# Optimization experiments

Hardware: AMD Instinct MI355X
Metric: run time of the kernel (lower is better)

The kernel has to match this reference:

```python
import jax, jax.numpy as jnp
import numpy as np

N_NODES = 100000
N_EDGES = 1600000
IN_C, HID_C, OUT_C = 128, 128, 64


def setup_inputs() -> dict:
    key = jax.random.key(0)
    k = jax.random.split(key, 5)
    x = jax.random.normal(k[0], (N_NODES, IN_C), dtype=jnp.float32)
    edge_index = jax.random.randint(k[1], (2, N_EDGES), 0, N_NODES, dtype=jnp.int32)
    # Glorot-ish scaling for the GCNConv linear weights
    W1 = jax.random.normal(k[2], (IN_C, HID_C), dtype=jnp.float32) * (1.0 / np.sqrt(IN_C))
    b1 = jnp.zeros((HID_C,), dtype=jnp.float32)
    W2 = jax.random.normal(k[3], (HID_C, OUT_C), dtype=jnp.float32) * (1.0 / np.sqrt(HID_C))
    b2 = jnp.zeros((OUT_C,), dtype=jnp.float32)
    return {"x": x, "edge_index": edge_index, "W1": W1, "b1": b1, "W2": W2, "b2": b2}


def _gcn_conv(h, W, b, src, dst, deg_inv_sqrt, n):
    # h: [N, F_in] -> linear transform, then deg-normalized scatter-add over edges
    h = h @ W  # [N, F_out]
    norm = deg_inv_sqrt[src] * deg_inv_sqrt[dst]  # [E+N] (self-loops included)
    msgs = h[src] * norm[:, None]  # gather + scale
    out = jax.ops.segment_sum(msgs, dst, num_segments=n)  # scatter-add to dst
    return out + b


def reference(x, edge_index, W1, b1, W2, b2):
    n = x.shape[0]
    loops = jnp.arange(n, dtype=edge_index.dtype)
    src = jnp.concatenate([edge_index[0], loops])  # add self-loops (PyG default)
    dst = jnp.concatenate([edge_index[1], loops])
    deg = jax.ops.segment_sum(jnp.ones_like(dst, dtype=x.dtype), dst, num_segments=n)
    deg_inv_sqrt = jax.lax.rsqrt(deg)  # deg >= 1 due to self-loops

    h = _gcn_conv(x, W1, b1, src, dst, deg_inv_sqrt, n)
    h = jax.nn.relu(h)
    # F.dropout(training=False) is identity at inference
    h = _gcn_conv(h, W2, b2, src, dst, deg_inv_sqrt, n)
    return jax.nn.log_softmax(h, axis=1)
```

## Files before the change

### kernel.cpp

```cpp
#include <hip/hip_runtime.h>
#include <hip/hip_bf16.h>


typedef unsigned short ushortT;
typedef unsigned char ucharT;
typedef __attribute__((ext_vector_type(8))) short short8v;
typedef __attribute__((ext_vector_type(4))) float float4v;
typedef __attribute__((ext_vector_type(2))) float float2v;
typedef __attribute__((ext_vector_type(8))) unsigned short ushort8v;

__device__ __forceinline__ float bf2f(ushortT u) {
  union { unsigned int i; float f; } x;
  x.i = ((unsigned int)u) << 16;
  return x.f;
}

__device__ __forceinline__ ushortT f2bf(float f) {
  __hip_bfloat16 h = __float2bfloat16(f);
  return *(ushortT*)&h;
}

__device__ __forceinline__ ucharT f2fp8(float f) {
  unsigned int w = __builtin_amdgcn_cvt_pk_fp8_f32(f, f, 0, false);
  return (ucharT)(w & 0xff);
}

__device__ __forceinline__ void fp8x8_to_f32(unsigned int lo, unsigned int hi,
                                             float* f) {
  float2v p0 = __builtin_amdgcn_cvt_pk_f32_fp8(lo, false);
  float2v p1 = __builtin_amdgcn_cvt_pk_f32_fp8(lo, true);
  float2v p2 = __builtin_amdgcn_cvt_pk_f32_fp8(hi, false);
  float2v p3 = __builtin_amdgcn_cvt_pk_f32_fp8(hi, true);
  f[0] = p0[0]; f[1] = p0[1]; f[2] = p1[0]; f[3] = p1[1];
  f[4] = p2[0]; f[5] = p2[1]; f[6] = p3[0]; f[7] = p3[1];
}

__device__ __forceinline__ void fp8x4_to_f32(unsigned int w, float* f) {
  float2v p0 = __builtin_amdgcn_cvt_pk_f32_fp8(w, false);
  float2v p1 = __builtin_amdgcn_cvt_pk_f32_fp8(w, true);
  f[0] = p0[0]; f[1] = p0[1]; f[2] = p1[0]; f[3] = p1[1];
}

__device__ __forceinline__ bool probe_isbf(const void* xv) {
  const ushortT* xr = (const ushortT*)xv;
  const int lane = threadIdx.x & 63;
  float v = bf2f(xr[lane]);
  bool sane = isfinite(v) && fabsf(v) < 1e4f;
  return __ballot(sane) == ~0ull;
}

__global__ __launch_bounds__(256) void bhist_k(const int* __restrict__ dst, int E, int B,
                                               int* __restrict__ gbc,
                                               const void* __restrict__ W1v,
                                               const void* __restrict__ W2v,
                                               const void* __restrict__ xv,
                                               ushortT* __restrict__ Wt1,
                                               ushortT* __restrict__ Wt2) {
  __shared__ int h[512];
  const int tid = threadIdx.x;
  const int gi = blockIdx.x * 256 + tid;
  if (gi < 24576) {
    const bool isbf = probe_isbf(xv);
    if (gi < 16384) {
      int nn = gi & 127, k = gi >> 7;
      ushortT v = isbf ? ((const ushortT*)W1v)[k * 128 + nn]
                       : f2bf(((const float*)W1v)[k * 128 + nn]);
      Wt1[nn * 128 + k] = v;
    } else {
      int j = gi - 16384;
      int nn = j & 63, k = j >> 6;
      ushortT v = isbf ? ((const ushortT*)W2v)[k * 64 + nn]
                       : f2bf(((const float*)W2v)[k * 64 + nn]);
      Wt2[nn * 128 + k] = v;
    }
  }
  for (int i = tid; i < B; i += 256) h[i] = 0;
  __syncthreads();
  const int i0 = blockIdx.x * 8192;
  const int iend = min(i0 + 8192, E);
  for (int i = i0 + tid; i < iend; i += 256) atomicAdd(&h[dst[i] >> 8], 1);
  __syncthreads();
  for (int i = tid; i < B; i += 256)
    if (h[i]) atomicAdd(&gbc[i], h[i]);
}

__global__ __launch_bounds__(256) void bscan_k(const int* __restrict__ gbc, int B,
                                               int* __restrict__ bbase,
                                               int* __restrict__ gcur) {
  __shared__ int p[256];
  const int t = threadIdx.x;
  int a = (2 * t < B) ? gbc[2 * t] : 0;
  int b = (2 * t + 1 < B) ? gbc[2 * t + 1] : 0;
  const int sum = a + b;
  p[t] = sum;
  __syncthreads();
  int run = sum;
  for (int off = 1; off < 256; off <<= 1) {
    int v = (t >= off) ? p[t - off] : 0;
    __syncthreads();
    run += v;
    p[t] = run;
    __syncthreads();
  }
  const int excl = run - sum;
  if (2 * t < B) { bbase[2 * t] = excl; gcur[2 * t] = excl; }
  if (2 * t + 1 < B) { bbase[2 * t + 1] = excl + a; gcur[2 * t + 1] = excl + a; }
}

__global__ __launch_bounds__(256) void bin_k(const int* __restrict__ srcv,
                                             const int* __restrict__ dstv, int E, int B,
                                             int* __restrict__ gcur,
                                             int* __restrict__ tmp) {
  __shared__ int hist[512];
  __shared__ int base[512];
  const int tid = threadIdx.x;
  const int i0 = blockIdx.x * 8192;
  const int iend = min(i0 + 8192, E);
  for (int i = tid; i < B; i += 256) hist[i] = 0;
  __syncthreads();
  for (int i = i0 + tid; i < iend; i += 256) atomicAdd(&hist[dstv[i] >> 8], 1);
  __syncthreads();
  for (int i = tid; i < B; i += 256) {
    int h = hist[i];
    base[i] = h ? atomicAdd(&gcur[i], h) : 0;
    hist[i] = 0;
  }
  __syncthreads();
  for (int i = i0 + tid; i < iend; i += 256) {
    int d = dstv[i];
    int s = srcv[i];
    int b = d >> 8;
    int l = atomicAdd(&hist[b], 1);
    tmp[base[b] + l] = s | ((d & 255) << 17);
  }
}

__global__ __launch_bounds__(256) void csr_k(const int* __restrict__ tmp,
                                             const int* __restrict__ bbase,
                                             const int* __restrict__ gbc, int n,
                                             int2* __restrict__ rpc,
                                             float* __restrict__ dis,
                                             int* __restrict__ col) {
  __shared__ int lhist[256];
  __shared__ int lexcl[256];
  const int b = blockIdx.x;
  const int tid = threadIdx.x;
  const int e0 = bbase[b];
  const int e1 = e0 + gbc[b];
  lhist[tid] = 0;
  __syncthreads();
  for (int i = e0 + tid; i < e1; i += 256) atomicAdd(&lhist[tmp[i] >> 17], 1);
  __syncthreads();
  const int v = lhist[tid];
  int run = v;
  lexcl[tid] = run;
  __syncthreads();
  for (int off = 1; off < 256; off <<= 1) {
    int t = (tid >= off) ? lexcl[tid - off] : 0;
    __syncthreads();
    run += t;
    lexcl[tid] = run;
    __syncthreads();
  }
  const int excl = run - v;
  const int node = (b << 8) + tid;
  if (node < n) {
    rpc[node] = make_int2(e0 + excl, v);
    dis[node] = rsqrtf((float)(v + 1));
  }
  lhist[tid] = 0;
  lexcl[tid] = excl;
  __syncthreads();
  for (int i = e0 + tid; i < e1; i += 256) {
    int p = tmp[i];
    int dloc = p >> 17;
    int s = p & 131071;
    int l = atomicAdd(&lhist[dloc], 1);
    col[e0 + lexcl[dloc] + l] = s;
  }
}

__global__ __launch_bounds__(512) void gemm1_k(const void* __restrict__ xv,
                                               const ushortT* __restrict__ Wt1,
                                               const float* __restrict__ dis,
                                               ucharT* __restrict__ Hb8, int n) {
  __shared__ ushortT sW[128 * 132];
  const bool isbf = probe_isbf(xv);
  const int tid = threadIdx.x;
  for (int i = tid; i < 4096; i += 512) {
    int nn = i >> 5, k4 = (i & 31) * 4;
    *(ushort4*)&sW[nn * 132 + k4] = *(const ushort4*)&Wt1[nn * 128 + k4];
  }
  __syncthreads();

  const int wave = tid >> 6;
  const int lane = tid & 63;
  const int m = lane & 15;
  const int quad = lane >> 4;
  const int row = blockIdx.x * 128 + wave * 16 + m;
  const int rowc = min(row, n - 1);

  float4v acc[8];
#pragma unroll
  for (int t = 0; t < 8; ++t) acc[t] = (float4v)(0.f);

  if (isbf) {
    const ushortT* xp = (const ushortT*)xv + (size_t)rowc * 128 + quad * 8;
#pragma unroll
    for (int kc = 0; kc < 4; ++kc) {
      short8v af = *(const short8v*)(xp + kc * 32);
#pragma unroll
      for (int nb = 0; nb < 8; ++nb) {
        short8v bf = *(const short8v*)&sW[(nb * 16 + m) * 132 + kc * 32 + quad * 8];
        acc[nb] = __builtin_amdgcn_mfma_f32_16x16x32_bf16(af, bf, acc[nb], 0, 0, 0);
      }
    }
  } else {
    const float* xp = (const float*)xv + (size_t)rowc * 128 + quad * 8;
#pragma unroll
    for (int kc = 0; kc < 4; ++kc) {
      float4 lo = *(const float4*)(xp + kc * 32);
      float4 hi = *(const float4*)(xp + kc * 32 + 4);
      short8v af;
      af[0] = (short)f2bf(lo.x); af[1] = (short)f2bf(lo.y);
      af[2] = (short)f2bf(lo.z); af[3] = (short)f2bf(lo.w);
      af[4] = (short)f2bf(hi.x); af[5] = (short)f2bf(hi.y);
      af[6] = (short)f2bf(hi.z); af[7] = (short)f2bf(hi.w);
#pragma unroll
      for (int nb = 0; nb < 8; ++nb) {
        short8v bf = *(const short8v*)&sW[(nb * 16 + m) * 132 + kc * 32 + quad * 8];
        acc[nb] = __builtin_amdgcn_mfma_f32_16x16x32_bf16(af, bf, acc[nb], 0, 0, 0);
      }
    }
  }

#pragma unroll
  for (int r = 0; r < 4; ++r) {
    int grow = blockIdx.x * 128 + wave * 16 + quad * 4 + r;
    if (grow <= n) {
      float sc = (grow < n) ? dis[grow] : 0.f;
#pragma unroll
      for (int nb = 0; nb < 8; ++nb)
        Hb8[(size_t)grow * 128 + nb * 16 + m] =
            (grow < n) ? f2fp8(sc * acc[nb][r]) : (ucharT)0;
    }
  }
}

__global__ __launch_bounds__(256) void agg1_k(const ucharT* __restrict__ Hb8,
                                              const int* __restrict__ col,
                                              const int2* __restrict__ rpc,
                                              const float* __restrict__ dis,
                                              const void* __restrict__ b1v,
                                              const void* __restrict__ xv,
                                              ushortT* __restrict__ Ab, int n) {
  const bool isbf = probe_isbf(xv);
  const int tid = threadIdx.x;
  const int lane = tid & 63;
  const int wave = tid >> 6;
  const int quad = lane >> 4;
  const int m = lane & 15;
  const int c8 = m * 8;
  const int node = blockIdx.x * 16 + wave * 4 + quad;
  const bool valid = node < n;
  const int nd = valid ? node : (n - 1);

  const int2 rc = rpc[nd];
  const int start = rc.x;
  const int cnt = valid ? rc.y : 0;
  const float din = dis[nd];

  const uint2 hsp = *(const uint2*)&Hb8[((unsigned)(valid ? node : n) << 7) + (unsigned)c8];
  float b[8];
  if (isbf) {
    ushort8v bb = *(const ushort8v*)((const ushortT*)b1v + c8);
#pragma unroll
    for (int k = 0; k < 8; ++k) b[k] = bf2f(bb[k]);
  } else {
    const float* bf = (const float*)b1v + c8;
#pragma unroll
    for (int k = 0; k < 8; ++k) b[k] = bf[k];
  }

  int cmax = cnt;
  cmax = max(cmax, __shfl_xor(cmax, 16));
  cmax = max(cmax, __shfl_xor(cmax, 32));
  const int cmaxs = __builtin_amdgcn_readfirstlane(cmax);

  float2v acc[4];
#pragma unroll
  for (int k = 0; k < 4; ++k) acc[k] = (float2v)(0.f);

  int nxt[8];
#pragma unroll
  for (int u = 0; u < 8; ++u) nxt[u] = col[start + u];
  for (int e = 0; e < cmaxs; e += 8) {
    int cur[8];
#pragma unroll
    for (int u = 0; u < 8; ++u) cur[u] = nxt[u];
#pragma unroll
    for (int u = 0; u < 8; ++u) nxt[u] = col[start + e + 8 + u];
#pragma unroll
    for (int u = 0; u < 8; ++u) {
      const int ee = e + u;
      int s = (ee < cnt) ? cur[u] : n;
      const uint2 h = *(const uint2*)&Hb8[((unsigned)s << 7) + (unsigned)c8];
      acc[0] += __builtin_amdgcn_cvt_pk_f32_fp8(h.x, false);
      acc[1] += __builtin_amdgcn_cvt_pk_f32_fp8(h.x, true);
      acc[2] += __builtin_amdgcn_cvt_pk_f32_fp8(h.y, false);
      acc[3] += __builtin_amdgcn_cvt_pk_f32_fp8(h.y, true);
    }
  }

  if (valid) {
    float hs[8];
    fp8x8_to_f32(hsp.x, hsp.y, hs);
    ushort8v o;
#pragma unroll
    for (int k = 0; k < 4; ++k) {
      o[2 * k]     = f2bf(fmaxf(fmaf(din, acc[k][0] + hs[2 * k],     b[2 * k]),     0.f));
      o[2 * k + 1] = f2bf(fmaxf(fmaf(din, acc[k][1] + hs[2 * k + 1], b[2 * k + 1]), 0.f));
    }
    *(ushort8v*)&Ab[(size_t)node * 128 + c8] = o;
  }
}

__global__ __launch_bounds__(512) void gemm2_k(const ushortT* __restrict__ Ab,
                                               const ushortT* __restrict__ Wt2,
                                               const float* __restrict__ dis,
                                               ucharT* __restrict__ H2b8, int n) {
  __shared__ ushortT sW[64 * 132];
  const int tid = threadIdx.x;
  for (int i = tid; i < 2048; i += 512) {
    int nn = i >> 5, k4 = (i & 31) * 4;
    *(ushort4*)&sW[nn * 132 + k4] = *(const ushort4*)&Wt2[nn * 128 + k4];
  }
  __syncthreads();

  const int wave = tid >> 6;
  const int lane = tid & 63;
  const int m = lane & 15;
  const int quad = lane >> 4;
  const int row = blockIdx.x * 128 + wave * 16 + m;
  const int rowc = min(row, n - 1);

  float4v acc[4];
#pragma unroll
  for (int t = 0; t < 4; ++t) acc[t] = (float4v)(0.f);

  const ushortT* ap = Ab + (size_t)rowc * 128 + quad * 8;
#pragma unroll
  for (int kc = 0; kc < 4; ++kc) {
    short8v af = *(const short8v*)(ap + kc * 32);
#pragma unroll
    for (int nb = 0; nb < 4; ++nb) {
      short8v bf = *(const short8v*)&sW[(nb * 16 + m) * 132 + kc * 32 + quad * 8];
      acc[nb] = __builtin_amdgcn_mfma_f32_16x16x32_bf16(af, bf, acc[nb], 0, 0, 0);
    }
  }

#pragma unroll
  for (int r = 0; r < 4; ++r) {
    int grow = blockIdx.x * 128 + wave * 16 + quad * 4 + r;
    if (grow <= n) {
      float sc = (grow < n) ? dis[grow] : 0.f;
#pragma unroll
      for (int nb = 0; nb < 4; ++nb)
        H2b8[(size_t)grow * 64 + nb * 16 + m] =
            (grow < n) ? f2fp8(sc * acc[nb][r]) : (ucharT)0;
    }
  }
}

__global__ __launch_bounds__(256) void agg2_k(const ucharT* __restrict__ H2b8,
                                              const int* __restrict__ col,
                                              const int2* __restrict__ rpc,
                                              const float* __restrict__ dis,
                                              const void* __restrict__ b2v,
                                              const void* __restrict__ xv,
                                              void* __restrict__ outv, int n) {
  const bool isbf = probe_isbf(xv);
  const int tid = threadIdx.x;
  const int lane = tid & 63;
  const int wave = tid >> 6;
  const int quad = lane >> 4;
  const int m = lane & 15;
  const int c4 = m * 4;
  const int node = blockIdx.x * 16 + wave * 4 + quad;
  const bool valid = node < n;
  const int nd = valid ? node : (n - 1);

  const int2 rc = rpc[nd];
  const int start = rc.x;
  const int cnt = valid ? rc.y : 0;
  const float din = dis[nd];

  const unsigned int hsp =
      *(const unsigned int*)&H2b8[((unsigned)(valid ? node : n) << 6) + (unsigned)c4];
  float b[4];
  if (isbf) {
    ushort4 bb = *(const ushort4*)((const ushortT*)b2v + c4);
    b[0] = bf2f(bb.x); b[1] = bf2f(bb.y); b[2] = bf2f(bb.z); b[3] = bf2f(bb.w);
  } else {
    const float* bf = (const float*)b2v + c4;
#pragma unroll
    for (int k = 0; k < 4; ++k) b[k] = bf[k];
  }

  int cmax = cnt;
  cmax = max(cmax, __shfl_xor(cmax, 16));
  cmax = max(cmax, __shfl_xor(cmax, 32));
  const int cmaxs = __builtin_amdgcn_readfirstlane(cmax);

  float2v acc[2];
  acc[0] = (float2v)(0.f);
  acc[1] = (float2v)(0.f);

  int nxt[8];
#pragma unroll
  for (int u = 0; u < 8; ++u) nxt[u] = col[start + u];
  for (int e = 0; e < cmaxs; e += 8) {
    int cur[8];
#pragma unroll
    for (int u = 0; u < 8; ++u) cur[u] = nxt[u];
#pragma unroll
    for (int u = 0; u < 8; ++u) nxt[u] = col[start + e + 8 + u];
#pragma unroll
    for (int u = 0; u < 8; ++u) {
      const int ee = e + u;
      int s = (ee < cnt) ? cur[u] : n;
      const unsigned int h = *(const unsigned int*)&H2b8[((unsigned)s << 6) + (unsigned)c4];
      acc[0] += __builtin_amdgcn_cvt_pk_f32_fp8(h, false);
      acc[1] += __builtin_amdgcn_cvt_pk_f32_fp8(h, true);
    }
  }

  float hs[4];
  fp8x4_to_f32(hsp, hs);
  float v[4];
  v[0] = fmaf(din, acc[0][0] + hs[0], b[0]);
  v[1] = fmaf(din, acc[0][1] + hs[1], b[1]);
  v[2] = fmaf(din, acc[1][0] + hs[2], b[2]);
  v[3] = fmaf(din, acc[1][1] + hs[3], b[3]);

  float mx = fmaxf(fmaxf(v[0], v[1]), fmaxf(v[2], v[3]));
  for (int off = 1; off < 16; off <<= 1) mx = fmaxf(mx, __shfl_xor(mx, off));
  float ssum = __expf(v[0] - mx) + __expf(v[1] - mx) + __expf(v[2] - mx) + __expf(v[3] - mx);
  for (int off = 1; off < 16; off <<= 1) ssum += __shfl_xor(ssum, off);
  const float lse = mx + __logf(ssum);

  if (valid) {
    if (isbf) {
      ushort4 o;
      o.x = f2bf(v[0] - lse); o.y = f2bf(v[1] - lse);
      o.z = f2bf(v[2] - lse); o.w = f2bf(v[3] - lse);
      *(ushort4*)((__hip_bfloat16*)outv + (size_t)node * 64 + c4) = o;
    } else {
      float4 o = make_float4(v[0] - lse, v[1] - lse, v[2] - lse, v[3] - lse);
      *(float4*)((float*)outv + (size_t)node * 64 + c4) = o;
    }
  }
}


extern "C" void kernel_launch(void* const* d_in, const int* in_sizes, int n_in,
                              void* d_out, int out_size, void* d_ws, size_t ws_size,
                              hipStream_t stream) {
  const void* x  = d_in[0];
  const int*  ei = (const int*)d_in[1];
  const void* W1 = d_in[2];
  const void* b1 = d_in[3];
  const void* W2 = d_in[4];
  const void* b2 = d_in[5];

  const int n = in_sizes[0] / 128;
  const int E = in_sizes[1] / 2;
  const int B = (n + 255) >> 8;
  const int* srcv = ei;
  const int* dstv = ei + E;

  char* p = (char*)d_ws;
  auto alloc = [&](size_t bytes) {
    char* q = p;
    p += (bytes + 255) & ~(size_t)255;
    return q;
  };
  ucharT* Hb8 = (ucharT*)alloc((size_t)(n + 1) * 128);
  ucharT* H2b8 = (ucharT*)alloc((size_t)(n + 1) * 64);
  ushortT* Ab = (ushortT*)alloc((size_t)n * 128 * 2);
  float* dis = (float*)alloc((size_t)n * 4);
  int2* rpc = (int2*)alloc((size_t)n * 8);
  int* gbc = (int*)alloc(512 * 4);
  int* bbase = (int*)alloc(512 * 4);
  int* gcur = (int*)alloc(512 * 4);
  ushortT* Wt1 = (ushortT*)alloc(16384 * 2);
  ushortT* Wt2 = (ushortT*)alloc(8192 * 2);
  int* tmp = (int*)alloc((size_t)E * 4);
  int* col = (int*)alloc(((size_t)E + 4096) * 4);

  (void)hipMemsetAsync(gbc, 0, 512 * sizeof(int), stream);

  const int gChunks = (E + 8191) / 8192;

  bhist_k<<<gChunks, 256, 0, stream>>>(dstv, E, B, gbc, W1, W2, x, Wt1, Wt2);
  bscan_k<<<1, 256, 0, stream>>>(gbc, B, bbase, gcur);
  bin_k<<<gChunks, 256, 0, stream>>>(srcv, dstv, E, B, gcur, tmp);
  csr_k<<<B, 256, 0, stream>>>(tmp, bbase, gbc, n, rpc, dis, col);

  gemm1_k<<<(n + 128) / 128, 512, 0, stream>>>(x, Wt1, dis, Hb8, n);
  agg1_k<<<(n + 15) / 16, 256, 0, stream>>>(Hb8, col, rpc, dis, b1, x, Ab, n);
  gemm2_k<<<(n + 128) / 128, 512, 0, stream>>>(Ab, Wt2, dis, H2b8, n);
  agg2_k<<<(n + 15) / 16, 256, 0, stream>>>(H2b8, col, rpc, dis, b2, x, d_out, n);
}
```

Before: 227.8 us.

## Drop scan kernel and split edges across half-waves in aggregation

Removes the separate single-block bucket-scan launch. Each bin_k block now recomputes the bucket prefix scan redundantly, each csr_k block reduces its own bucket offset, and gcur is zeroed inside bhist_k. Separately, both aggregation kernels now assign two half-groups of 8 lanes to each node. Each lane loads twice as many fp8 feature bytes per gather while the half-groups take alternate edges, and the partial sums are combined with a cross-lane shuffle. This aims to cut launch overhead and raise memory-level parallelism per gather, at the cost of redundant scan work per block and extra shuffles.

Measured after the change: 229.7 us. About the same (+0.8%).

```diff
diff --git a/kernel.cpp b/kernel.cpp
--- a/kernel.cpp
+++ b/kernel.cpp
@@ -25,22 +25,6 @@
   return (ucharT)(w & 0xff);
 }
 
-__device__ __forceinline__ void fp8x8_to_f32(unsigned int lo, unsigned int hi,
-                                             float* f) {
-  float2v p0 = __builtin_amdgcn_cvt_pk_f32_fp8(lo, false);
-  float2v p1 = __builtin_amdgcn_cvt_pk_f32_fp8(lo, true);
-  float2v p2 = __builtin_amdgcn_cvt_pk_f32_fp8(hi, false);
-  float2v p3 = __builtin_amdgcn_cvt_pk_f32_fp8(hi, true);
-  f[0] = p0[0]; f[1] = p0[1]; f[2] = p1[0]; f[3] = p1[1];
-  f[4] = p2[0]; f[5] = p2[1]; f[6] = p3[0]; f[7] = p3[1];
-}
-
-__device__ __forceinline__ void fp8x4_to_f32(unsigned int w, float* f) {
-  float2v p0 = __builtin_amdgcn_cvt_pk_f32_fp8(w, false);
-  float2v p1 = __builtin_amdgcn_cvt_pk_f32_fp8(w, true);
-  f[0] = p0[0]; f[1] = p0[1]; f[2] = p1[0]; f[3] = p1[1];
-}
-
 __device__ __forceinline__ bool probe_isbf(const void* xv) {
   const ushortT* xr = (const ushortT*)xv;
   const int lane = threadIdx.x & 63;
@@ -55,9 +39,12 @@
                                                const void* __restrict__ W2v,
                                                const void* __restrict__ xv,
                                                ushortT* __restrict__ Wt1,
-                                               ushortT* __restrict__ Wt2) {
+                                               ushortT* __restrict__ Wt2,
+                                               int* __restrict__ gcur) {
   __shared__ int h[512];
   const int tid = threadIdx.x;
+  if (blockIdx.x == 0)
+    for (int i = tid; i < 512; i += 256) gcur[i] = 0;
   const int gi = blockIdx.x * 256 + tid;
   if (gi < 24576) {
     const bool isbf = probe_isbf(xv);
@@ -84,36 +71,34 @@
     if (h[i]) atomicAdd(&gbc[i], h[i]);
 }
 
-__global__ __launch_bounds__(256) void bscan_k(const int* __restrict__ gbc, int B,
-                                               int* __restrict__ bbase,
-                                               int* __restrict__ gcur) {
-  __shared__ int p[256];
-  const int t = threadIdx.x;
-  int a = (2 * t < B) ? gbc[2 * t] : 0;
-  int b = (2 * t + 1 < B) ? gbc[2 * t + 1] : 0;
-  const int sum = a + b;
-  p[t] = sum;
-  __syncthreads();
-  int run = sum;
-  for (int off = 1; off < 256; off <<= 1) {
-    int v = (t >= off) ? p[t - off] : 0;
-    __syncthreads();
-    run += v;
-    p[t] = run;
-    __syncthreads();
-  }
-  const int excl = run - sum;
-  if (2 * t < B) { bbase[2 * t] = excl; gcur[2 * t] = excl; }
-  if (2 * t + 1 < B) { bbase[2 * t + 1] = excl + a; gcur[2 * t + 1] = excl + a; }
-}
-
 __global__ __launch_bounds__(256) void bin_k(const int* __restrict__ srcv,
                                              const int* __restrict__ dstv, int E, int B,
+                                             const int* __restrict__ gbc,
                                              int* __restrict__ gcur,
                                              int* __restrict__ tmp) {
   __shared__ int hist[512];
   __shared__ int base[512];
-  const int tid = threadIdx.x;
+  __shared__ int sbb[512];
+  const int tid = threadIdx.x;
+  {
+    int a = (2 * tid < B) ? gbc[2 * tid] : 0;
+    int b2 = (2 * tid + 1 < B) ? gbc[2 * tid + 1] : 0;
+    const int sum = a + b2;
+    hist[tid] = sum;
+    __syncthreads();
+    int run = sum;
+    for (int off = 1; off < 256; off <<= 1) {
+      int v = (tid >= off) ? hist[tid - off] : 0;
+      __syncthreads();
+      run += v;
+      hist[tid] = run;
+      __syncthreads();
+    }
+    const int excl = run - sum;
+    if (2 * tid < B) sbb[2 * tid] = excl;
+    if (2 * tid + 1 < B) sbb[2 * tid + 1] = excl + a;
+    __syncthreads();
+  }
   const int i0 = blockIdx.x * 8192;
   const int iend = min(i0 + 8192, E);
   for (int i = tid; i < B; i += 256) hist[i] = 0;
@@ -122,7 +107,7 @@
   __syncthreads();
   for (int i = tid; i < B; i += 256) {
     int h = hist[i];
-    base[i] = h ? atomicAdd(&gcur[i], h) : 0;
+    base[i] = h ? (sbb[i] + atomicAdd(&gcur[i], h)) : 0;
     hist[i] = 0;
   }
   __syncthreads();
@@ -136,17 +121,26 @@
 }
 
 __global__ __launch_bounds__(256) void csr_k(const int* __restrict__ tmp,
-                                             const int* __restrict__ bbase,
                                              const int* __restrict__ gbc, int n,
                                              int2* __restrict__ rpc,
                                              float* __restrict__ dis,
                                              int* __restrict__ col) {
   __shared__ int lhist[256];
   __shared__ int lexcl[256];
+  __shared__ int red[256];
   const int b = blockIdx.x;
   const int tid = threadIdx.x;
-  const int e0 = bbase[b];
+  int part = 0;
+  for (int i = tid; i < b; i += 256) part += gbc[i];
+  red[tid] = part;
+  __syncthreads();
+  for (int off = 128; off > 0; off >>= 1) {
+    if (tid < off) red[tid] += red[tid + off];
+    __syncthreads();
+  }
+  const int e0 = red[0];
   const int e1 = e0 + gbc[b];
+  __syncthreads();
   lhist[tid] = 0;
   __syncthreads();
   for (int i = e0 + tid; i < e1; i += 256) atomicAdd(&lhist[tmp[i] >> 17], 1);
@@ -259,8 +253,8 @@
   const int lane = tid & 63;
   const int wave = tid >> 6;
   const int quad = lane >> 4;
-  const int m = lane & 15;
-  const int c8 = m * 8;
+  const int o = (lane >> 3) & 1;
+  const int c16 = (lane & 7) * 16;
   const int node = blockIdx.x * 16 + wave * 4 + quad;
   const bool valid = node < n;
   const int nd = valid ? node : (n - 1);
@@ -270,16 +264,17 @@
   const int cnt = valid ? rc.y : 0;
   const float din = dis[nd];
 
-  const uint2 hsp = *(const uint2*)&Hb8[((unsigned)(valid ? node : n) << 7) + (unsigned)c8];
-  float b[8];
+  const uint4 hsp = *(const uint4*)&Hb8[((unsigned)(valid ? node : n) << 7) + (unsigned)c16];
+  float b[16];
   if (isbf) {
-    ushort8v bb = *(const ushort8v*)((const ushortT*)b1v + c8);
-#pragma unroll
-    for (int k = 0; k < 8; ++k) b[k] = bf2f(bb[k]);
+    ushort8v b0 = *(const ushort8v*)((const ushortT*)b1v + c16);
+    ushort8v b1 = *(const ushort8v*)((const ushortT*)b1v + c16 + 8);
+#pragma unroll
+    for (int k = 0; k < 8; ++k) { b[k] = bf2f(b0[k]); b[8 + k] = bf2f(b1[k]); }
   } else {
-    const float* bf = (const float*)b1v + c8;
-#pragma unroll
-    for (int k = 0; k < 8; ++k) b[k] = bf[k];
+    const float* bf = (const float*)b1v + c16;
+#pragma unroll
+    for (int k = 0; k < 16; ++k) b[k] = bf[k];
   }
 
   int cmax = cnt;
@@ -287,41 +282,68 @@
   cmax = max(cmax, __shfl_xor(cmax, 32));
   const int cmaxs = __builtin_amdgcn_readfirstlane(cmax);
 
-  float2v acc[4];
-#pragma unroll
-  for (int k = 0; k < 4; ++k) acc[k] = (float2v)(0.f);
-
-  int nxt[8];
-#pragma unroll
-  for (int u = 0; u < 8; ++u) nxt[u] = col[start + u];
+  float2v acc[8];
+#pragma unroll
+  for (int k = 0; k < 8; ++k) acc[k] = (float2v)(0.f);
+
+  int nxt[4];
+#pragma unroll
+  for (int u = 0; u < 4; ++u) nxt[u] = col[start + 2 * u + o];
   for (int e = 0; e < cmaxs; e += 8) {
-    int cur[8];
-#pragma unroll
-    for (int u = 0; u < 8; ++u) cur[u] = nxt[u];
-#pragma unroll
-    for (int u = 0; u < 8; ++u) nxt[u] = col[start + e + 8 + u];
-#pragma unroll
-    for (int u = 0; u < 8; ++u) {
-      const int ee = e + u;
+    int cur[4];
+#pragma unroll
+    for (int u = 0; u < 4; ++u) cur[u] = nxt[u];
+#pragma unroll
+    for (int u = 0; u < 4; ++u) nxt[u] = col[start + e + 8 + 2 * u + o];
+#pragma unroll
+    for (int u = 0; u < 4; ++u) {
+      const int ee = e + 2 * u + o;
       int s = (ee < cnt) ? cur[u] : n;
-      const uint2 h = *(const uint2*)&Hb8[((unsigned)s << 7) + (unsigned)c8];
+      const uint4 h = *(const uint4*)&Hb8[((unsigned)s << 7) + (unsigned)c16];
       acc[0] += __builtin_amdgcn_cvt_pk_f32_fp8(h.x, false);
       acc[1] += __builtin_amdgcn_cvt_pk_f32_fp8(h.x, true);
       acc[2] += __builtin_amdgcn_cvt_pk_f32_fp8(h.y, false);
       acc[3] += __builtin_amdgcn_cvt_pk_f32_fp8(h.y, true);
-    }
-  }
-
-  if (valid) {
-    float hs[8];
-    fp8x8_to_f32(hsp.x, hsp.y, hs);
-    ushort8v o;
+      acc[4] += __builtin_amdgcn_cvt_pk_f32_fp8(h.z, false);
+      acc[5] += __builtin_amdgcn_cvt_pk_f32_fp8(h.z, true);
+      acc[6] += __builtin_amdgcn_cvt_pk_f32_fp8(h.w, false);
+      acc[7] += __builtin_amdgcn_cvt_pk_f32_fp8(h.w, true);
+    }
+  }
+
+#pragma unroll
+  for (int k = 0; k < 8; ++k) {
+    float t0 = __shfl_xor(acc[k][0], 8);
+    float t1 = __shfl_xor(acc[k][1], 8);
+    acc[k][0] += t0;
+    acc[k][1] += t1;
+  }
+
+  if (valid && o == 0) {
+    float hs[16];
+    {
+      const unsigned int w4[4] = {hsp.x, hsp.y, hsp.z, hsp.w};
+#pragma unroll
+      for (int w = 0; w < 4; ++w) {
+        float2v p0 = __builtin_amdgcn_cvt_pk_f32_fp8(w4[w], false);
+        float2v p1 = __builtin_amdgcn_cvt_pk_f32_fp8(w4[w], true);
+        hs[4 * w] = p0[0]; hs[4 * w + 1] = p0[1];
+        hs[4 * w + 2] = p1[0]; hs[4 * w + 3] = p1[1];
+      }
+    }
+    ushort8v o0, o1;
 #pragma unroll
     for (int k = 0; k < 4; ++k) {
-      o[2 * k]     = f2bf(fmaxf(fmaf(din, acc[k][0] + hs[2 * k],     b[2 * k]),     0.f));
-      o[2 * k + 1] = f2bf(fmaxf(fmaf(din, acc[k][1] + hs[2 * k + 1], b[2 * k + 1]), 0.f));
-    }
-    *(ushort8v*)&Ab[(size_t)node * 128 + c8] = o;
+      o0[2 * k]     = f2bf(fmaxf(fmaf(din, acc[k][0] + hs[2 * k],     b[2 * k]),     0.f));
+      o0[2 * k + 1] = f2bf(fmaxf(fmaf(din, acc[k][1] + hs[2 * k + 1], b[2 * k + 1]), 0.f));
+    }
+#pragma unroll
+    for (int k = 4; k < 8; ++k) {
+      o1[2 * (k - 4)]     = f2bf(fmaxf(fmaf(din, acc[k][0] + hs[2 * k],     b[2 * k]),     0.f));
+      o1[2 * (k - 4) + 1] = f2bf(fmaxf(fmaf(din, acc[k][1] + hs[2 * k + 1], b[2 * k + 1]), 0.f));
+    }
+    *(ushort8v*)&Ab[(size_t)node * 128 + c16] = o0;
+    *(ushort8v*)&Ab[(size_t)node * 128 + c16 + 8] = o1;
   }
 }
 
@@ -384,8 +406,8 @@
   const int lane = tid & 63;
   const int wave = tid >> 6;
   const int quad = lane >> 4;
-  const int m = lane & 15;
-  const int c4 = m * 4;
+  const int o = (lane >> 3) & 1;
+  const int c8 = (lane & 7) * 8;
   const int node = blockIdx.x * 16 + wave * 4 + quad;
   const bool valid = node < n;
   const int nd = valid ? node : (n - 1);
@@ -395,16 +417,17 @@
   const int cnt = valid ? rc.y : 0;
   const float din = dis[nd];
 
-  const unsigned int hsp =
-      *(const unsigned int*)&H2b8[((unsigned)(valid ? node : n) << 6) + (unsigned)c4];
-  float b[4];
+  const uint2 hsp =
+      *(const uint2*)&H2b8[((unsigned)(valid ? node : n) << 6) + (unsigned)c8];
+  float b[8];
   if (isbf) {
-    ushort4 bb = *(const ushort4*)((const ushortT*)b2v + c4);
-    b[0] = bf2f(bb.x); b[1] = bf2f(bb.y); b[2] = bf2f(bb.z); b[3] = bf2f(bb.w);
+    ushort8v bb = *(const ushort8v*)((const ushortT*)b2v + c8);
+#pragma unroll
+    for (int k = 0; k < 8; ++k) b[k] = bf2f(bb[k]);
   } else {
-    const float* bf = (const float*)b2v + c4;
-#pragma unroll
-    for (int k = 0; k < 4; ++k) b[k] = bf[k];
+    const float* bf = (const float*)b2v + c8;
+#pragma unroll
+    for (int k = 0; k < 8; ++k) b[k] = bf[k];
   }
 
   int cmax = cnt;
@@ -412,52 +435,76 @@
   cmax = max(cmax, __shfl_xor(cmax, 32));
   const int cmaxs = __builtin_amdgcn_readfirstlane(cmax);
 
-  float2v acc[2];
-  acc[0] = (float2v)(0.f);
-  acc[1] = (float2v)(0.f);
-
-  int nxt[8];
-#pragma unroll
-  for (int u = 0; u < 8; ++u) nxt[u] = col[start + u];
+  float2v acc[4];
+#pragma unroll
+  for (int k = 0; k < 4; ++k) acc[k] = (float2v)(0.f);
+
+  int nxt[4];
+#pragma unroll
+  for (int u = 0; u < 4; ++u) nxt[u] = col[start + 2 * u + o];
   for (int e = 0; e < cmaxs; e += 8) {
-    int cur[8];
-#pragma unroll
-    for (int u = 0; u < 8; ++u) cur[u] = nxt[u];
-#pragma unroll
-    for (int u = 0; u < 8; ++u) nxt[u] = col[start + e + 8 + u];
-#pragma unroll
-    for (int u = 0; u < 8; ++u) {
-      const int ee = e + u;
+    int cur[4];
+#pragma unroll
+    for (int u = 0; u < 4; ++u) cur[u] = nxt[u];
+#pragma unroll
+    for (int u = 0; u < 4; ++u) nxt[u] = col[start + e + 8 + 2 * u + o];
+#pragma unroll
+    for (int u = 0; u < 4; ++u) {
+      const int ee = e + 2 * u + o;
       int s = (ee < cnt) ? cur[u] : n;
-      const unsigned int h = *(const unsigned int*)&H2b8[((unsigned)s << 6) + (unsigned)c4];
-      acc[0] += __builtin_amdgcn_cvt_pk_f32_fp8(h, false);
-      acc[1] += __builtin_amdgcn_cvt_pk_f32_fp8(h, true);
-    }
-  }
-
-  float hs[4];
-  fp8x4_to_f32(hsp, hs);
-  float v[4];
-  v[0] = fmaf(din, acc[0][0] + hs[0], b[0]);
-  v[1] = fmaf(din, acc[0][1] + hs[1], b[1]);
-  v[2] = fmaf(din, acc[1][0] + hs[2], b[2]);
-  v[3] = fmaf(din, acc[1][1] + hs[3], b[3]);
-
-  float mx = fmaxf(fmaxf(v[0], v[1]), fmaxf(v[2], v[3]));
-  for (int off = 1; off < 16; off <<= 1) mx = fmaxf(mx, __shfl_xor(mx, off));
-  float ssum = __expf(v[0] - mx) + __expf(v[1] - mx) + __expf(v[2] - mx) + __expf(v[3] - mx);
-  for (int off = 1; off < 16; off <<= 1) ssum += __shfl_xor(ssum, off);
+      const uint2 h = *(const uint2*)&H2b8[((unsigned)s << 6) + (unsigned)c8];
+      acc[0] += __builtin_amdgcn_cvt_pk_f32_fp8(h.x, false);
+      acc[1] += __builtin_amdgcn_cvt_pk_f32_fp8(h.x, true);
+      acc[2] += __builtin_amdgcn_cvt_pk_f32_fp8(h.y, false);
+      acc[3] += __builtin_amdgcn_cvt_pk_f32_fp8(h.y, true);
+    }
+  }
+
+#pragma unroll
+  for (int k = 0; k < 4; ++k) {
+    float t0 = __shfl_xor(acc[k][0], 8);
+    float t1 = __shfl_xor(acc[k][1], 8);
+    acc[k][0] += t0;
+    acc[k][1] += t1;
+  }
+
+  float hs[8];
+  {
+    float2v p0 = __builtin_amdgcn_cvt_pk_f32_fp8(hsp.x, false);
+    float2v p1 = __builtin_amdgcn_cvt_pk_f32_fp8(hsp.x, true);
+    float2v p2 = __builtin_amdgcn_cvt_pk_f32_fp8(hsp.y, false);
+    float2v p3 = __builtin_amdgcn_cvt_pk_f32_fp8(hsp.y, true);
+    hs[0] = p0[0]; hs[1] = p0[1]; hs[2] = p1[0]; hs[3] = p1[1];
+    hs[4] = p2[0]; hs[5] = p2[1]; hs[6] = p3[0]; hs[7] = p3[1];
+  }
+  float v[8];
+#pragma unroll
+  for (int k = 0; k < 4; ++k) {
+    v[2 * k]     = fmaf(din, acc[k][0] + hs[2 * k],     b[2 * k]);
+    v[2 * k + 1] = fmaf(din, acc[k][1] + hs[2 * k + 1], b[2 * k + 1]);
+  }
+
+  float mx = v[0];
+#pragma unroll
+  for (int k = 1; k < 8; ++k) mx = fmaxf(mx, v[k]);
+  for (int off = 1; off < 8; off <<= 1) mx = fmaxf(mx, __shfl_xor(mx, off));
+  float ssum = 0.f;
+#pragma unroll
+  for (int k = 0; k < 8; ++k) ssum += __expf(v[k] - mx);
+  for (int off = 1; off < 8; off <<= 1) ssum += __shfl_xor(ssum, off);
   const float lse = mx + __logf(ssum);
 
-  if (valid) {
+  if (valid && o == 0) {
     if (isbf) {
-      ushort4 o;
-      o.x = f2bf(v[0] - lse); o.y = f2bf(v[1] - lse);
-      o.z = f2bf(v[2] - lse); o.w = f2bf(v[3] - lse);
-      *(ushort4*)((__hip_bfloat16*)outv + (size_t)node * 64 + c4) = o;
+      ushort8v ov;
+#pragma unroll
+      for (int k = 0; k < 8; ++k) ov[k] = f2bf(v[k] - lse);
+      *(ushort8v*)((__hip_bfloat16*)outv + (size_t)node * 64 + c8) = ov;
     } else {
-      float4 o = make_float4(v[0] - lse, v[1] - lse, v[2] - lse, v[3] - lse);
-      *(float4*)((float*)outv + (size_t)node * 64 + c4) = o;
+      float4 o0 = make_float4(v[0] - lse, v[1] - lse, v[2] - lse, v[3] - lse);
+      float4 o1 = make_float4(v[4] - lse, v[5] - lse, v[6] - lse, v[7] - lse);
+      *(float4*)((float*)outv + (size_t)node * 64 + c8) = o0;
+      *(float4*)((float*)outv + (size_t)node * 64 + c8 + 4) = o1;
     }
   }
 }
@@ -491,7 +538,6 @@
   float* dis = (float*)alloc((size_t)n * 4);
   int2* rpc = (int2*)alloc((size_t)n * 8);
   int* gbc = (int*)alloc(512 * 4);
-  int* bbase = (int*)alloc(512 * 4);
   int* gcur = (int*)alloc(512 * 4);
   ushortT* Wt1 = (ushortT*)alloc(16384 * 2);
   ushortT* Wt2 = (ushortT*)alloc(8192 * 2);
@@ -502,10 +548,9 @@
 
   const int gChunks = (E + 8191) / 8192;
 
-  bhist_k<<<gChunks, 256, 0, stream>>>(dstv, E, B, gbc, W1, W2, x, Wt1, Wt2);
-  bscan_k<<<1, 256, 0, stream>>>(gbc, B, bbase, gcur);
-  bin_k<<<gChunks, 256, 0, stream>>>(srcv, dstv, E, B, gcur, tmp);
-  csr_k<<<B, 256, 0, stream>>>(tmp, bbase, gbc, n, rpc, dis, col);
+  bhist_k<<<gChunks, 256, 0, stream>>>(dstv, E, B, gbc, W1, W2, x, Wt1, Wt2, gcur);
+  bin_k<<<gChunks, 256, 0, stream>>>(srcv, dstv, E, B, gbc, gcur, tmp);
+  csr_k<<<B, 256, 0, stream>>>(tmp, gbc, n, rpc, dis, col);
 
   gemm1_k<<<(n + 128) / 128, 512, 0, stream>>>(x, Wt1, dis, Hb8, n);
   agg1_k<<<(n + 15) / 16, 256, 0, stream>>>(Hb8, col, rpc, dis, b1, x, Ab, n);
```
